# Performance work log

Measured on AMD Instinct MI355X. Metric: run time of the kernel, lower is better.

Reference implementation:

```python
import jax, jax.numpy as jnp
import numpy as np

HIDDEN = 2048
HEAD_DIM = 256
N_HEADS = 8
N_KV_HEADS = 2
N_GROUPS = N_HEADS // N_KV_HEADS
EPS = 1e-6
WAVELENGTH = 10000.0
ROPE_SCALE = 1.0
NEG_INF = -1e9


def setup_inputs() -> dict:
    key = jax.random.key(0)
    ks = jax.random.split(key, 8)
    B, S = 2, 2048
    hidden_states = jax.random.normal(ks[0], (B, S, HIDDEN), dtype=jnp.float32)
    # additive causal mask: 0 on/below diagonal, -1e9 above
    causal = jnp.tril(jnp.ones((S, S), dtype=bool))
    attention_mask = jnp.where(causal, 0.0, NEG_INF).astype(jnp.float32)[None, None]
    attention_mask = jnp.broadcast_to(attention_mask, (B, 1, S, S))
    sd = 1.0 / np.sqrt(HIDDEN)
    wq = jax.random.normal(ks[1], (HIDDEN, N_HEADS * HEAD_DIM), dtype=jnp.float32) * sd
    wk = jax.random.normal(ks[2], (HIDDEN, N_KV_HEADS * HEAD_DIM), dtype=jnp.float32) * sd
    wv = jax.random.normal(ks[3], (HIDDEN, N_KV_HEADS * HEAD_DIM), dtype=jnp.float32) * sd
    wo = jax.random.normal(ks[4], (N_HEADS * HEAD_DIM, HIDDEN), dtype=jnp.float32) * (1.0 / np.sqrt(N_HEADS * HEAD_DIM))
    q_scale = 1.0 + 0.02 * jax.random.normal(ks[5], (HEAD_DIM,), dtype=jnp.float32)
    k_scale = 1.0 + 0.02 * jax.random.normal(ks[6], (HEAD_DIM,), dtype=jnp.float32)
    return {"hidden_states": hidden_states, "attention_mask": attention_mask,
            "wq": wq, "wk": wk, "wv": wv, "wo": wo,
            "q_scale": q_scale, "k_scale": k_scale}


def _rms_norm(x, scale=None):
    # Gemma3nRMSNorm: compute in float32, optional scale, cast back
    x32 = x.astype(jnp.float32)
    out = x32 * jax.lax.rsqrt(jnp.mean(x32 * x32, axis=-1, keepdims=True) + EPS)
    if scale is not None:
        out = out * scale.astype(jnp.float32)
    return out.astype(x.dtype)


def _rope(x, start_index=0):
    # x: [B, S, H, D]; keras-hub RotaryEmbedding (half-split rotate)
    S, D = x.shape[1], x.shape[-1]
    inv_freq = 1.0 / (WAVELENGTH ** (jnp.arange(0, D, 2, dtype=jnp.float32) / D))
    pos = (jnp.arange(S, dtype=jnp.float32) + start_index) / ROPE_SCALE
    freq = jnp.einsum("s,f->sf", pos, inv_freq)           # [S, D/2]
    emb = jnp.concatenate([freq, freq], axis=-1)          # [S, D]
    cos = jnp.cos(emb)[None, :, None, :].astype(x.dtype)
    sin = jnp.sin(emb)[None, :, None, :].astype(x.dtype)
    x1, x2 = jnp.split(x, 2, axis=-1)
    rot = jnp.concatenate([-x2, x1], axis=-1)
    return x * cos + rot * sin


def reference(hidden_states, attention_mask, wq, wk, wv, wo, q_scale, k_scale):
    B, S, _ = hidden_states.shape
    q = (hidden_states @ wq).reshape(B, S, N_HEADS, HEAD_DIM)
    k = (hidden_states @ wk).reshape(B, S, N_KV_HEADS, HEAD_DIM)
    v = (hidden_states @ wv).reshape(B, S, N_KV_HEADS, HEAD_DIM)
    q = _rope(_rms_norm(q, q_scale))
    k = _rope(_rms_norm(k, k_scale))
    v = _rms_norm(v)  # with_scale=False
    # GQA: repeat KV heads, then BHSD layout
    k = jnp.repeat(k, N_GROUPS, axis=2)
    v = jnp.repeat(v, N_GROUPS, axis=2)
    q = q.transpose(0, 2, 1, 3)
    k = k.transpose(0, 2, 1, 3)
    v = v.transpose(0, 2, 1, 3)
    scores = jnp.einsum("bhqd,bhkd->bhqk", q, k) / np.sqrt(HEAD_DIM)
    scores = scores + attention_mask.astype(scores.dtype)
    probs = jax.nn.softmax(scores.astype(jnp.float32), axis=-1).astype(hidden_states.dtype)
    out = jnp.einsum("bhqk,bhkd->bhqd", probs, v)
    out = out.transpose(0, 2, 1, 3).reshape(B, S, N_HEADS * HEAD_DIM)
    return out @ wo
```

## Files before the change

### kernel.cpp

```cpp
#include <hip/hip_runtime.h>
#include <cstdint>
#include <cstddef>

#define SEQ   2048
#define BATCH 2
#define NH    8
#define NKV   2
#define DH    256
#define HID   2048
#define MR    (BATCH*SEQ)

typedef _Float16 h8 __attribute__((ext_vector_type(8)));
typedef _Float16 h4 __attribute__((ext_vector_type(4)));
typedef float   f32x4 __attribute__((ext_vector_type(4)));
typedef int     i32x4 __attribute__((ext_vector_type(4)));

__device__ __forceinline__ f32x4 mfma16(h8 a, h8 b, f32x4 c) {
  return __builtin_amdgcn_mfma_f32_16x16x32_f16(a, b, c, 0, 0, 0);
}
__device__ __forceinline__ void gload16(const void* g, void* l) {
  __builtin_amdgcn_global_load_lds((__attribute__((address_space(1))) void*)g,
                                   (__attribute__((address_space(3))) void*)l,
                                   16, 0, 0);
}
__device__ __forceinline__ int pkf16(float a, float b) {
  auto t = __builtin_amdgcn_cvt_pkrtz(a, b);
  return __builtin_bit_cast(int, t);
}

__global__ __launch_bounds__(256) void cvt_f16(const float* __restrict__ in,
                                               _Float16* __restrict__ out, int n4) {
  const int i = blockIdx.x * 256 + threadIdx.x;
  if (i >= n4) return;
  const float4 v = ((const float4*)in)[i];
  h4 o = { (_Float16)v.x, (_Float16)v.y, (_Float16)v.z, (_Float16)v.w };
  ((h4*)out)[i] = o;
}

__global__ __launch_bounds__(256) void wtrans(const float* __restrict__ in,
                                              _Float16* __restrict__ out,
                                              int N, int K) {
  __shared__ float L[32][33];
  const int n0 = blockIdx.x * 32, k0 = blockIdx.y * 32;
  const int t = threadIdx.x;
  const int r = t >> 3, c4 = (t & 7) * 4;
  const float4 v = *(const float4*)&in[(size_t)(k0 + r) * N + n0 + c4];
  L[r][c4] = v.x; L[r][c4 + 1] = v.y; L[r][c4 + 2] = v.z; L[r][c4 + 3] = v.w;
  __syncthreads();
  h4 o = { (_Float16)L[c4][r], (_Float16)L[c4 + 1][r],
           (_Float16)L[c4 + 2][r], (_Float16)L[c4 + 3][r] };
  *(h4*)&out[(size_t)(n0 + r) * K + k0 + c4] = o;
}

__global__ __launch_bounds__(256) void gemm_f16(const _Float16* __restrict__ A,
                                                const _Float16* __restrict__ Bt,
                                                float* __restrict__ C,
                                                const int N, const int K) {
  __shared__ __align__(16) unsigned char sm[32768];
  const int t = threadIdx.x, w = t >> 6, lane = t & 63;
  const int l15 = lane & 15, l4 = lane >> 4;
  const int wr = w >> 1, wc = w & 1;
  const int m0 = blockIdx.y * 128, n0 = blockIdx.x * 128;
  const int swz = (l15 & 7) << 4;
  const size_t rb = (size_t)K * 2;

  int rS[4], cS[4];
#pragma unroll
  for (int i = 0; i < 4; ++i) {
    const int o = i * 4096 + w * 1024 + lane * 16;
    rS[i] = o >> 7;
    cS[i] = (o & 127) ^ ((rS[i] & 7) << 4);
  }
  const char* Ab = (const char*)A + (size_t)m0 * rb;
  const char* Bb = (const char*)Bt + (size_t)n0 * rb;

  f32x4 acc[4][4] = {};

  for (int k0 = 0; k0 < K; k0 += 64) {
    __syncthreads();
#pragma unroll
    for (int i = 0; i < 4; ++i) {
      gload16(Ab + (size_t)rS[i] * rb + k0 * 2 + cS[i], sm + i * 4096 + w * 1024);
      gload16(Bb + (size_t)rS[i] * rb + k0 * 2 + cS[i], sm + 16384 + i * 4096 + w * 1024);
    }
    __syncthreads();
#pragma unroll
    for (int kk = 0; kk < 2; ++kk) {
      const int ko = (kk * 64 + l4 * 16) ^ swz;
      h8 av[4], bv[4];
#pragma unroll
      for (int f = 0; f < 4; ++f) {
        av[f] = *(const h8*)(sm + (wr * 64 + f * 16 + l15) * 128 + ko);
        bv[f] = *(const h8*)(sm + 16384 + (wc * 64 + f * 16 + l15) * 128 + ko);
      }
#pragma unroll
      for (int i = 0; i < 4; ++i)
#pragma unroll
        for (int j = 0; j < 4; ++j)
          acc[i][j] = mfma16(av[i], bv[j], acc[i][j]);
    }
  }
#pragma unroll
  for (int i = 0; i < 4; ++i)
#pragma unroll
    for (int r = 0; r < 4; ++r) {
      const int row = m0 + wr * 64 + i * 16 + l4 * 4 + r;
      float* Cp = C + (size_t)row * N + n0 + wc * 64 + l15;
#pragma unroll
      for (int j = 0; j < 4; ++j) Cp[j * 16] = acc[i][j][r];
    }
}

__global__ __launch_bounds__(256) void norm_rope_q(const float* __restrict__ QKVp,
                                                   _Float16* __restrict__ Qh,
                                                   const float* __restrict__ q_scale) {
  const int idx = blockIdx.x;
  const int t = threadIdx.x;
  const int h = idx & 7;
  const int bs = idx >> 3;
  const int s = bs & (SEQ - 1);
  const int b = bs >> 11;
  const float x = QKVp[(size_t)bs * 3072 + h * 256 + t];
  float ss = x * x;
#pragma unroll
  for (int off = 32; off; off >>= 1) ss += __shfl_xor(ss, off);
  __shared__ float red[4];
  if ((t & 63) == 0) red[t >> 6] = ss;
  __syncthreads();
  const float tot = red[0] + red[1] + red[2] + red[3];
  const float inv = rsqrtf(tot * (1.0f / 256.0f) + 1e-6f);
  const float xn = x * inv * q_scale[t];
  __shared__ float rowbuf[256];
  rowbuf[t] = xn;
  __syncthreads();
  const int f = t & 127;
  const float invf = expf(-0.07195578415606391f * (float)f);
  float sn, cs;
  sincosf((float)s * invf, &sn, &cs);
  const float other = rowbuf[t ^ 128];
  const float o = (t < 128) ? (xn * cs - other * sn) : (xn * cs + other * sn);
  Qh[((size_t)(b * NH + h) * SEQ + s) * DH + t] = (_Float16)(o * 0.0625f);
}

__global__ __launch_bounds__(256) void norm_kv(const float* __restrict__ QKVp,
                                               _Float16* __restrict__ Kh,
                                               _Float16* __restrict__ Vh,
                                               const float* __restrict__ k_scale) {
  const int idx = blockIdx.x;
  const int t = threadIdx.x;
  const bool isK = idx < 8192;
  const int i = isK ? idx : idx - 8192;
  const int kv = i & 1;
  const int bs = i >> 1;
  const int s = bs & (SEQ - 1);
  const int b = bs >> 11;
  const int col = (isK ? 2048 + kv * DH : 2560 + kv * DH) + t;
  const float x = QKVp[(size_t)bs * 3072 + col];
  float ss = x * x;
#pragma unroll
  for (int off = 32; off; off >>= 1) ss += __shfl_xor(ss, off);
  __shared__ float red[4];
  if ((t & 63) == 0) red[t >> 6] = ss;
  __syncthreads();
  const float tot = red[0] + red[1] + red[2] + red[3];
  const float inv = rsqrtf(tot * (1.0f / 256.0f) + 1e-6f);
  float xn = x * inv;
  const size_t o = ((size_t)(b * NKV + kv) * SEQ + s) * DH + t;
  if (isK) {
    xn *= k_scale[t];
    __shared__ float rowbuf[256];
    rowbuf[t] = xn;
    __syncthreads();
    const int f = t & 127;
    const float invf = expf(-0.07195578415606391f * (float)f);
    float sn, cs;
    sincosf((float)s * invf, &sn, &cs);
    const float other = rowbuf[t ^ 128];
    const float ov = (t < 128) ? (xn * cs - other * sn) : (xn * cs + other * sn);
    Kh[o] = (_Float16)ov;
  } else {
    Vh[o] = (_Float16)xn;
  }
}

__global__ __launch_bounds__(256) void transpose_v(const _Float16* __restrict__ Vh,
                                                   _Float16* __restrict__ Vt) {
  __shared__ _Float16 L[32][36];
  const int s0 = blockIdx.x * 32, d0 = blockIdx.y * 32;
  const size_t base = (size_t)blockIdx.z * SEQ * DH;
  const int t = threadIdx.x;
  const int r = t >> 3, c4 = (t & 7) * 4;
  const h4 v = *(const h4*)&Vh[base + (size_t)(s0 + r) * DH + d0 + c4];
  L[r][c4] = v.x; L[r][c4 + 1] = v.y; L[r][c4 + 2] = v.z; L[r][c4 + 3] = v.w;
  __syncthreads();
  h4 o = { L[c4][r], L[c4 + 1][r], L[c4 + 2][r], L[c4 + 3][r] };
  *(h4*)&Vt[base + (size_t)(d0 + r) * SEQ + s0 + c4] = o;
}

__global__ __launch_bounds__(256, 1) void attn_f16(const _Float16* __restrict__ Qh,
                                                   const _Float16* __restrict__ Kh,
                                                   const _Float16* __restrict__ Vt,
                                                   _Float16* __restrict__ Ah) {
  __shared__ __align__(16) unsigned char sm[65536];
  const int qt = blockIdx.x;
  const int h = blockIdx.y, b = blockIdx.z;
  const int kh = h >> 2;
  const int q0 = qt * 128;
  const int nt = 4 * (qt + 1);
  const int t = threadIdx.x, w = t >> 6, lane = t & 63;
  const int l15 = lane & 15, l4 = lane >> 4;
  const int swzk = (l15 & 7) << 4;
  const int swzv = (l15 & 3) << 4;

  const char* Qg = (const char*)(Qh + (size_t)(b * NH + h) * SEQ * DH);
  const char* Kg = (const char*)(Kh + (size_t)(b * NKV + kh) * SEQ * DH);
  const char* Vg = (const char*)(Vt + (size_t)(b * NKV + kh) * DH * SEQ);

  auto stage_tile = [&](int kt, int p) {
    unsigned char* Kb = sm + p * 32768;
    unsigned char* Vb = Kb + 16384;
#pragma unroll
    for (int i = 0; i < 4; ++i) {
      const int o = i * 4096 + w * 1024 + lane * 16;
      const int row = o >> 9;
      const int koff = (o & 511) ^ ((row & 7) << 4);
      gload16(Kg + (size_t)(kt * 32 + row) * 512 + koff, Kb + i * 4096 + w * 1024);
      const int d = o >> 6;
      const int voff = (o & 63) ^ ((d & 3) << 4);
      gload16(Vg + (size_t)d * (SEQ * 2) + kt * 64 + voff, Vb + i * 4096 + w * 1024);
    }
  };

  stage_tile(0, 0);

  h8 qf[2][8];
#pragma unroll
  for (int g = 0; g < 2; ++g) {
    const int qrow = q0 + w * 32 + g * 16 + l15;
#pragma unroll
    for (int dc = 0; dc < 8; ++dc)
      qf[g][dc] = *(const h8*)(Qg + (size_t)qrow * 512 + dc * 64 + l4 * 16);
  }

  f32x4 o_acc[2][16] = {};
  float mrun[2] = { -3e38f, -3e38f };
  float lrun[2] = { 0.f, 0.f };
  __syncthreads();

  for (int kt = 0; kt < nt; ++kt) {
    const int p = kt & 1;
    if (kt + 1 < nt) stage_tile(kt + 1, p ^ 1);

    if (kt * 32 <= q0 + w * 32 + 31) {
      const unsigned char* Kb = sm + p * 32768;
      const unsigned char* Vb = Kb + 16384;

      f32x4 sc[2][2];
#pragma unroll
      for (int fk = 0; fk < 2; ++fk) {
        f32x4 a0 = {}, a1 = {};
        const int krow = fk * 16 + l15;
#pragma unroll
        for (int dc = 0; dc < 8; ++dc) {
          const h8 kf = *(const h8*)(Kb + krow * 512 + ((dc * 64 + l4 * 16) ^ swzk));
          a0 = mfma16(kf, qf[0][dc], a0);
          a1 = mfma16(kf, qf[1][dc], a1);
        }
        sc[0][fk] = a0; sc[1][fk] = a1;
      }

      h8 pa[2];
#pragma unroll
      for (int g = 0; g < 2; ++g) {
        const int qlo = q0 + w * 32 + g * 16;
        const int qrow = qlo + l15;
        float e[2][4];
        if (kt * 32 + 31 > qlo) {
#pragma unroll
          for (int fk = 0; fk < 2; ++fk)
#pragma unroll
            for (int r = 0; r < 4; ++r)
              e[fk][r] = (kt * 32 + fk * 16 + l4 * 4 + r <= qrow) ? sc[g][fk][r]
                                                                  : -3e38f;
        } else {
#pragma unroll
          for (int fk = 0; fk < 2; ++fk)
#pragma unroll
            for (int r = 0; r < 4; ++r) e[fk][r] = sc[g][fk][r];
        }
        float pm = -3e38f;
#pragma unroll
        for (int fk = 0; fk < 2; ++fk)
#pragma unroll
          for (int r = 0; r < 4; ++r) pm = fmaxf(pm, e[fk][r]);
        pm = fmaxf(pm, __shfl_xor(pm, 16));
        pm = fmaxf(pm, __shfl_xor(pm, 32));
        const float mnew = fmaxf(mrun[g], pm);
        const float alpha = __expf(mrun[g] - mnew);
        mrun[g] = mnew;
        float ls = 0.f;
#pragma unroll
        for (int fk = 0; fk < 2; ++fk)
#pragma unroll
          for (int r = 0; r < 4; ++r) {
            e[fk][r] = __expf(e[fk][r] - mnew);
            ls += e[fk][r];
          }
        ls += __shfl_xor(ls, 16);
        ls += __shfl_xor(ls, 32);
        lrun[g] = lrun[g] * alpha + ls;

        float al[4];
#pragma unroll
        for (int r = 0; r < 4; ++r) al[r] = __shfl(alpha, l4 * 4 + r);
#pragma unroll
        for (int fd = 0; fd < 16; ++fd)
#pragma unroll
          for (int r = 0; r < 4; ++r) o_acc[g][fd][r] *= al[r];

        const int d0 = pkf16(e[0][0], e[0][1]);
        const int d1 = pkf16(e[0][2], e[0][3]);
        const int d2 = pkf16(e[1][0], e[1][1]);
        const int d3 = pkf16(e[1][2], e[1][3]);
        const int src0 = l15 + ((l4 & 1) << 5);
        const int src1 = src0 + 16;
        const bool lowk = (l4 < 2);
        const int s00 = __shfl(d0, src0);
        const int s10 = __shfl(d1, src0);
        const int s20 = __shfl(d2, src0);
        const int s30 = __shfl(d3, src0);
        const int s01 = __shfl(d0, src1);
        const int s11 = __shfl(d1, src1);
        const int s21 = __shfl(d2, src1);
        const int s31 = __shfl(d3, src1);
        i32x4 pw = { lowk ? s00 : s20, lowk ? s10 : s30,
                     lowk ? s01 : s21, lowk ? s11 : s31 };
        pa[g] = __builtin_bit_cast(h8, pw);
      }

      const int ko = (l4 * 16) ^ swzv;
#pragma unroll
      for (int fd = 0; fd < 16; ++fd) {
        const h8 vf = *(const h8*)(Vb + (fd * 16 + l15) * 64 + ko);
        o_acc[0][fd] = mfma16(pa[0], vf, o_acc[0][fd]);
        o_acc[1][fd] = mfma16(pa[1], vf, o_acc[1][fd]);
      }
    }
    __syncthreads();
  }

#pragma unroll
  for (int g = 0; g < 2; ++g) {
    const float inv = 1.0f / lrun[g];
#pragma unroll
    for (int r = 0; r < 4; ++r) {
      const float linv = __shfl(inv, l4 * 4 + r);
      const int srow = q0 + w * 32 + g * 16 + l4 * 4 + r;
      _Float16* Op = Ah + (size_t)(b * SEQ + srow) * (NH * DH) + h * DH + l15;
#pragma unroll
      for (int fd = 0; fd < 16; ++fd)
        Op[fd * 16] = (_Float16)(o_acc[g][fd][r] * linv);
    }
  }
}

extern "C" void kernel_launch(void* const* d_in, const int* in_sizes, int n_in,
                              void* d_out, int out_size, void* d_ws, size_t ws_size,
                              hipStream_t stream) {
  (void)in_sizes; (void)n_in; (void)out_size; (void)ws_size;
  const float* hidden  = (const float*)d_in[0];
  const float* wq      = (const float*)d_in[2];
  const float* wk      = (const float*)d_in[3];
  const float* wv      = (const float*)d_in[4];
  const float* wo      = (const float*)d_in[5];
  const float* q_scale = (const float*)d_in[6];
  const float* k_scale = (const float*)d_in[7];
  float* out = (float*)d_out;

  uint8_t* ws = (uint8_t*)d_ws;
  _Float16* hid_h = (_Float16*)ws;  ws += (size_t)MR * HID * 2;
  _Float16* Wt    = (_Float16*)ws;  ws += (size_t)3072 * HID * 2;
  float*    QKVp  = (float*)ws;     ws += (size_t)MR * 3072 * 4;
  _Float16* Qh    = (_Float16*)ws;  ws += (size_t)MR * HID * 2;
  _Float16* Kh    = (_Float16*)ws;  ws += (size_t)MR * 512 * 2;
  _Float16* Vh    = (_Float16*)ws;  ws += (size_t)MR * 512 * 2;
  _Float16* Vt    = (_Float16*)ws;  ws += (size_t)MR * 512 * 2;
  _Float16* Ah    = (_Float16*)QKVp;

  const dim3 blk(256);
  cvt_f16<<<dim3(8192), blk, 0, stream>>>(hidden, hid_h, MR * HID / 4);
  wtrans<<<dim3(64, 64), blk, 0, stream>>>(wq, Wt, 2048, 2048);
  wtrans<<<dim3(16, 64), blk, 0, stream>>>(wk, Wt + (size_t)2048 * 2048, 512, 2048);
  wtrans<<<dim3(16, 64), blk, 0, stream>>>(wv, Wt + (size_t)2560 * 2048, 512, 2048);
  gemm_f16<<<dim3(24, 32), blk, 0, stream>>>(hid_h, Wt, QKVp, 3072, 2048);
  wtrans<<<dim3(64, 64), blk, 0, stream>>>(wo, Wt, 2048, 2048);
  norm_rope_q<<<dim3(32768), blk, 0, stream>>>(QKVp, Qh, q_scale);
  norm_kv<<<dim3(16384), blk, 0, stream>>>(QKVp, Kh, Vh, k_scale);
  transpose_v<<<dim3(64, 8, 4), blk, 0, stream>>>(Vh, Vt);
  attn_f16<<<dim3(16, 8, 2), blk, 0, stream>>>(Qh, Kh, Vt, Ah);
  gemm_f16<<<dim3(16, 32), blk, 0, stream>>>(Ah, Wt, out, 2048, 2048);
}
```

Baseline: 473.0 us.

## Precompute RoPE table, shrink attention blocks, add lazy rescale and priority hints

Adds a kernel that precomputes a cos/sin table once per sequence position, so the norm kernels load from it instead of calling expf and sincosf per element. The attention kernel moves to 128-thread blocks over 64-row query tiles, doubling the grid. Query tiles for the second batch run in reverse order to spread the causal workload. K and V fragments are hoisted into registers before the MFMA loops, with s_setprio around them, and the K swizzle widens to 16 rows. The online-softmax rescale of the output accumulator is skipped unless the running max grows by more than 8, which saves ALU work but raises register pressure.

```diff
diff --git a/kernel.cpp b/kernel.cpp
--- a/kernel.cpp
+++ b/kernel.cpp
@@ -111,9 +111,18 @@
     }
 }
 
+__global__ __launch_bounds__(128) void rope_tab(float2* __restrict__ tab) {
+  const int s = blockIdx.x, f = threadIdx.x;
+  const float invf = expf(-0.07195578415606391f * (float)f);
+  float sn, cs;
+  sincosf((float)s * invf, &sn, &cs);
+  tab[(size_t)s * 128 + f] = make_float2(cs, sn);
+}
+
 __global__ __launch_bounds__(256) void norm_rope_q(const float* __restrict__ QKVp,
                                                    _Float16* __restrict__ Qh,
-                                                   const float* __restrict__ q_scale) {
+                                                   const float* __restrict__ q_scale,
+                                                   const float2* __restrict__ tab) {
   const int idx = blockIdx.x;
   const int t = threadIdx.x;
   const int h = idx & 7;
@@ -133,19 +142,18 @@
   __shared__ float rowbuf[256];
   rowbuf[t] = xn;
   __syncthreads();
-  const int f = t & 127;
-  const float invf = expf(-0.07195578415606391f * (float)f);
-  float sn, cs;
-  sincosf((float)s * invf, &sn, &cs);
+  const float2 cst = tab[(size_t)s * 128 + (t & 127)];
   const float other = rowbuf[t ^ 128];
-  const float o = (t < 128) ? (xn * cs - other * sn) : (xn * cs + other * sn);
+  const float o = (t < 128) ? (xn * cst.x - other * cst.y)
+                            : (xn * cst.x + other * cst.y);
   Qh[((size_t)(b * NH + h) * SEQ + s) * DH + t] = (_Float16)(o * 0.0625f);
 }
 
 __global__ __launch_bounds__(256) void norm_kv(const float* __restrict__ QKVp,
                                                _Float16* __restrict__ Kh,
                                                _Float16* __restrict__ Vh,
-                                               const float* __restrict__ k_scale) {
+                                               const float* __restrict__ k_scale,
+                                               const float2* __restrict__ tab) {
   const int idx = blockIdx.x;
   const int t = threadIdx.x;
   const bool isK = idx < 8192;
@@ -171,12 +179,10 @@
     __shared__ float rowbuf[256];
     rowbuf[t] = xn;
     __syncthreads();
-    const int f = t & 127;
-    const float invf = expf(-0.07195578415606391f * (float)f);
-    float sn, cs;
-    sincosf((float)s * invf, &sn, &cs);
+    const float2 cst = tab[(size_t)s * 128 + (t & 127)];
     const float other = rowbuf[t ^ 128];
-    const float ov = (t < 128) ? (xn * cs - other * sn) : (xn * cs + other * sn);
+    const float ov = (t < 128) ? (xn * cst.x - other * cst.y)
+                               : (xn * cst.x + other * cst.y);
     Kh[o] = (_Float16)ov;
   } else {
     Vh[o] = (_Float16)xn;
@@ -197,19 +203,20 @@
   *(h4*)&Vt[base + (size_t)(d0 + r) * SEQ + s0 + c4] = o;
 }
 
-__global__ __launch_bounds__(256, 1) void attn_f16(const _Float16* __restrict__ Qh,
+__global__ __launch_bounds__(128, 1) void attn_f16(const _Float16* __restrict__ Qh,
                                                    const _Float16* __restrict__ Kh,
                                                    const _Float16* __restrict__ Vt,
                                                    _Float16* __restrict__ Ah) {
   __shared__ __align__(16) unsigned char sm[65536];
-  const int qt = blockIdx.x;
+  const int pid = blockIdx.x;
   const int h = blockIdx.y, b = blockIdx.z;
   const int kh = h >> 2;
-  const int q0 = qt * 128;
-  const int nt = 4 * (qt + 1);
+  const int qt = b ? (31 - pid) : pid;
+  const int q0 = qt * 64;
+  const int nt = 2 * (qt + 1);
   const int t = threadIdx.x, w = t >> 6, lane = t & 63;
   const int l15 = lane & 15, l4 = lane >> 4;
-  const int swzk = (l15 & 7) << 4;
+  const int swzk = l15 << 4;
   const int swzv = (l15 & 3) << 4;
 
   const char* Qg = (const char*)(Qh + (size_t)(b * NH + h) * SEQ * DH);
@@ -220,14 +227,14 @@
     unsigned char* Kb = sm + p * 32768;
     unsigned char* Vb = Kb + 16384;
 #pragma unroll
-    for (int i = 0; i < 4; ++i) {
-      const int o = i * 4096 + w * 1024 + lane * 16;
+    for (int i = 0; i < 8; ++i) {
+      const int o = i * 2048 + w * 1024 + lane * 16;
       const int row = o >> 9;
-      const int koff = (o & 511) ^ ((row & 7) << 4);
-      gload16(Kg + (size_t)(kt * 32 + row) * 512 + koff, Kb + i * 4096 + w * 1024);
+      const int koff = (o & 511) ^ ((row & 15) << 4);
+      gload16(Kg + (size_t)(kt * 32 + row) * 512 + koff, Kb + i * 2048 + w * 1024);
       const int d = o >> 6;
       const int voff = (o & 63) ^ ((d & 3) << 4);
-      gload16(Vg + (size_t)d * (SEQ * 2) + kt * 64 + voff, Vb + i * 4096 + w * 1024);
+      gload16(Vg + (size_t)d * (SEQ * 2) + kt * 64 + voff, Vb + i * 2048 + w * 1024);
     }
   };
 
@@ -255,33 +262,41 @@
       const unsigned char* Kb = sm + p * 32768;
       const unsigned char* Vb = Kb + 16384;
 
-      f32x4 sc[2][2];
-#pragma unroll
-      for (int fk = 0; fk < 2; ++fk) {
-        f32x4 a0 = {}, a1 = {};
-        const int krow = fk * 16 + l15;
+      h8 kf[2][8];
+#pragma unroll
+      for (int fk = 0; fk < 2; ++fk)
+#pragma unroll
+        for (int dc = 0; dc < 8; ++dc)
+          kf[fk][dc] = *(const h8*)(Kb + (fk * 16 + l15) * 512 +
+                                    ((dc * 64 + l4 * 16) ^ swzk));
+      f32x4 sc[2][2] = {};
+      __builtin_amdgcn_s_setprio(1);
+#pragma unroll
+      for (int fk = 0; fk < 2; ++fk)
 #pragma unroll
         for (int dc = 0; dc < 8; ++dc) {
-          const h8 kf = *(const h8*)(Kb + krow * 512 + ((dc * 64 + l4 * 16) ^ swzk));
-          a0 = mfma16(kf, qf[0][dc], a0);
-          a1 = mfma16(kf, qf[1][dc], a1);
+          sc[0][fk] = mfma16(kf[fk][dc], qf[0][dc], sc[0][fk]);
+          sc[1][fk] = mfma16(kf[fk][dc], qf[1][dc], sc[1][fk]);
         }
-        sc[0][fk] = a0; sc[1][fk] = a1;
-      }
+      __builtin_amdgcn_s_setprio(0);
+
+      h8 vf[16];
+#pragma unroll
+      for (int fd = 0; fd < 16; ++fd)
+        vf[fd] = *(const h8*)(Vb + (fd * 16 + l15) * 64 + ((l4 * 16) ^ swzv));
 
       h8 pa[2];
 #pragma unroll
       for (int g = 0; g < 2; ++g) {
         const int qlo = q0 + w * 32 + g * 16;
-        const int qrow = qlo + l15;
         float e[2][4];
         if (kt * 32 + 31 > qlo) {
 #pragma unroll
           for (int fk = 0; fk < 2; ++fk)
 #pragma unroll
             for (int r = 0; r < 4; ++r)
-              e[fk][r] = (kt * 32 + fk * 16 + l4 * 4 + r <= qrow) ? sc[g][fk][r]
-                                                                  : -3e38f;
+              e[fk][r] = (kt * 32 + fk * 16 + l4 * 4 + r <= qlo + l15)
+                             ? sc[g][fk][r] : -3e38f;
         } else {
 #pragma unroll
           for (int fk = 0; fk < 2; ++fk)
@@ -295,28 +310,32 @@
           for (int r = 0; r < 4; ++r) pm = fmaxf(pm, e[fk][r]);
         pm = fmaxf(pm, __shfl_xor(pm, 16));
         pm = fmaxf(pm, __shfl_xor(pm, 32));
-        const float mnew = fmaxf(mrun[g], pm);
-        const float alpha = __expf(mrun[g] - mnew);
-        mrun[g] = mnew;
+        float alpha = 1.0f;
+        float mb = mrun[g];
+        if (!__all(pm - mrun[g] <= 8.0f)) {
+          const float mnew = fmaxf(mrun[g], pm);
+          alpha = __expf(mrun[g] - mnew);
+          mrun[g] = mnew;
+          mb = mnew;
+          float al[4];
+#pragma unroll
+          for (int r = 0; r < 4; ++r) al[r] = __shfl(alpha, l4 * 4 + r);
+#pragma unroll
+          for (int fd = 0; fd < 16; ++fd)
+#pragma unroll
+            for (int r = 0; r < 4; ++r) o_acc[g][fd][r] *= al[r];
+        }
         float ls = 0.f;
 #pragma unroll
         for (int fk = 0; fk < 2; ++fk)
 #pragma unroll
           for (int r = 0; r < 4; ++r) {
-            e[fk][r] = __expf(e[fk][r] - mnew);
+            e[fk][r] = __expf(e[fk][r] - mb);
             ls += e[fk][r];
           }
         ls += __shfl_xor(ls, 16);
         ls += __shfl_xor(ls, 32);
         lrun[g] = lrun[g] * alpha + ls;
-
-        float al[4];
-#pragma unroll
-        for (int r = 0; r < 4; ++r) al[r] = __shfl(alpha, l4 * 4 + r);
-#pragma unroll
-        for (int fd = 0; fd < 16; ++fd)
-#pragma unroll
-          for (int r = 0; r < 4; ++r) o_acc[g][fd][r] *= al[r];
 
         const int d0 = pkf16(e[0][0], e[0][1]);
         const int d1 = pkf16(e[0][2], e[0][3]);
@@ -338,13 +357,13 @@
         pa[g] = __builtin_bit_cast(h8, pw);
       }
 
-      const int ko = (l4 * 16) ^ swzv;
+      __builtin_amdgcn_s_setprio(1);
 #pragma unroll
       for (int fd = 0; fd < 16; ++fd) {
-        const h8 vf = *(const h8*)(Vb + (fd * 16 + l15) * 64 + ko);
-        o_acc[0][fd] = mfma16(pa[0], vf, o_acc[0][fd]);
-        o_acc[1][fd] = mfma16(pa[1], vf, o_acc[1][fd]);
+        o_acc[0][fd] = mfma16(pa[0], vf[fd], o_acc[0][fd]);
+        o_acc[1][fd] = mfma16(pa[1], vf[fd], o_acc[1][fd]);
       }
+      __builtin_amdgcn_s_setprio(0);
     }
     __syncthreads();
   }
@@ -385,18 +404,20 @@
   _Float16* Kh    = (_Float16*)ws;  ws += (size_t)MR * 512 * 2;
   _Float16* Vh    = (_Float16*)ws;  ws += (size_t)MR * 512 * 2;
   _Float16* Vt    = (_Float16*)ws;  ws += (size_t)MR * 512 * 2;
+  float2*   tab   = (float2*)ws;    ws += (size_t)SEQ * 128 * 8;
   _Float16* Ah    = (_Float16*)QKVp;
 
   const dim3 blk(256);
   cvt_f16<<<dim3(8192), blk, 0, stream>>>(hidden, hid_h, MR * HID / 4);
+  rope_tab<<<dim3(SEQ), dim3(128), 0, stream>>>(tab);
   wtrans<<<dim3(64, 64), blk, 0, stream>>>(wq, Wt, 2048, 2048);
   wtrans<<<dim3(16, 64), blk, 0, stream>>>(wk, Wt + (size_t)2048 * 2048, 512, 2048);
   wtrans<<<dim3(16, 64), blk, 0, stream>>>(wv, Wt + (size_t)2560 * 2048, 512, 2048);
   gemm_f16<<<dim3(24, 32), blk, 0, stream>>>(hid_h, Wt, QKVp, 3072, 2048);
   wtrans<<<dim3(64, 64), blk, 0, stream>>>(wo, Wt, 2048, 2048);
-  norm_rope_q<<<dim3(32768), blk, 0, stream>>>(QKVp, Qh, q_scale);
-  norm_kv<<<dim3(16384), blk, 0, stream>>>(QKVp, Kh, Vh, k_scale);
+  norm_rope_q<<<dim3(32768), blk, 0, stream>>>(QKVp, Qh, q_scale, tab);
+  norm_kv<<<dim3(16384), blk, 0, stream>>>(QKVp, Kh, Vh, k_scale, tab);
   transpose_v<<<dim3(64, 8, 4), blk, 0, stream>>>(Vh, Vt);
-  attn_f16<<<dim3(16, 8, 2), blk, 0, stream>>>(Qh, Kh, Vt, Ah);
+  attn_f16<<<dim3(32, 8, 2), dim3(128), 0, stream>>>(Qh, Kh, Vt, Ah);
   gemm_f16<<<dim3(16, 32), blk, 0, stream>>>(Ah, Wt, out, 2048, 2048);
 }
```

Measured after the change: 450.6 us. 1.05x faster.
